# Optimization experiments

Measured on AMD Instinct MI355X. Metric: run time of the kernel, lower is better.

Reference implementation:

```python
import jax, jax.numpy as jnp
import numpy as np

B, SEQ, DIM, D, K = 32, 2048, 512, 512, 128


def _ln(x, g, b, eps=1e-5):
    m = x.mean(-1, keepdims=True)
    v = ((x - m) ** 2).mean(-1, keepdims=True)
    return (x - m) / jnp.sqrt(v + eps) * g + b


def _gelu(v):
    return jax.nn.gelu(v, approximate=False)


def _diff_topk(s, k, t):
    # s: (B, N) scores; iterative relaxed top-k (Xie & Ermon style).
    def step(carry, _):
        a = jax.nn.softmax(carry / t, axis=-1)
        carry = carry + jnp.log(jnp.clip(1.0 - a, 1e-6, 1.0))
        return carry, a
    _, Ws = jax.lax.scan(step, s, None, length=k)  # (k, B, N)
    return jnp.transpose(Ws, (1, 0, 2))            # (B, k, N)


def setup_inputs():
    key = jax.random.key(0)
    ks = jax.random.split(key, 6)
    w = lambda k_, shape: jax.random.normal(k_, shape, dtype=jnp.float32) * 0.02
    return {
        'x': jax.random.normal(ks[0], (B, SEQ, DIM), dtype=jnp.float32),
        'tau': jnp.array(0.0, dtype=jnp.float32),
        'ln1_g': jnp.ones((DIM,), jnp.float32), 'ln1_b': jnp.zeros((DIM,), jnp.float32),
        'W1': w(ks[1], (DIM, D)), 'b1': jnp.zeros((D,), jnp.float32),
        'ln2_g': jnp.ones((SEQ,), jnp.float32), 'ln2_b': jnp.zeros((SEQ,), jnp.float32),
        'W2': w(ks[2], (SEQ, SEQ)), 'b2': jnp.zeros((SEQ,), jnp.float32),
        'ln3_g': jnp.ones((D,), jnp.float32), 'ln3_b': jnp.zeros((D,), jnp.float32),
        'W3': w(ks[3], (D, D + 1)), 'b3': jnp.zeros((D + 1,), jnp.float32),
        'ln4_g': jnp.ones((D,), jnp.float32), 'ln4_b': jnp.zeros((D,), jnp.float32),
        'W4': w(ks[4], (D, DIM)), 'b4': jnp.zeros((DIM,), jnp.float32),
    }


def reference(x, tau, ln1_g, ln1_b, W1, b1, ln2_g, ln2_b, W2, b2,
              ln3_g, ln3_b, W3, b3, ln4_g, ln4_b, W4, b4):
    # tok_proj: LN(dim) -> Linear(dim, D) -> GELU
    x_tok = _gelu(_ln(x, ln1_g, ln1_b) @ W1 + b1)                  # (B, N, D)
    # ch_proj over the token axis: LN(seq) -> Linear(seq, seq) -> GELU
    xt = jnp.swapaxes(x_tok, 1, 2)                                  # (B, D, N)
    x_ch = jnp.swapaxes(_gelu(_ln(xt, ln2_g, ln2_b) @ W2 + b2), 1, 2)
    # proj -> split score | features
    h = _ln(x_tok + x_ch, ln3_g, ln3_b) @ W3 + b3                   # (B, N, D+1)
    x_score, x_proj = h[..., 0], h[..., 1:]
    t = jax.nn.sigmoid(jnp.clip(tau, -2.0, 5.0))
    Wmat = _diff_topk(x_score, K, t)                                # (B, k, N)
    Z = jnp.einsum('bkn,bnd->bkd', Wmat, x_proj)                    # soft gather
    Y = jnp.einsum('bkn,bkd->bnd', Wmat, Z)                         # soft scatter
    return _ln(x_proj + Y, ln4_g, ln4_b) @ W4 + b4                  # (B, N, dim)
```

## Files before the change

### kernel.cpp

```cpp
#include <hip/hip_runtime.h>
#include <math.h>

#define B_   32
#define SEQ_ 2048
#define DIM_ 512
#define KSEL 128

typedef _Float16 f16;
typedef _Float16 half8 __attribute__((ext_vector_type(8)));
typedef _Float16 half4 __attribute__((ext_vector_type(4)));
typedef float floatx4 __attribute__((ext_vector_type(4)));

#define LSTR2 32

__device__ __forceinline__ float gelu_exact(float v) {
  return 0.5f * v * (1.0f + erff(v * 0.70710678118654752440f));
}

__global__ __launch_bounds__(256) void rowstats512(const float* __restrict__ X,
                                                   float* __restrict__ mean,
                                                   float* __restrict__ rstd) {
  int row = blockIdx.x * 4 + (threadIdx.x >> 6);
  int l = threadIdx.x & 63;
  const float4* p = (const float4*)(X + (size_t)row * 512);
  float4 v0 = p[l * 2], v1 = p[l * 2 + 1];
  float s = v0.x + v0.y + v0.z + v0.w + v1.x + v1.y + v1.z + v1.w;
  float q = v0.x*v0.x + v0.y*v0.y + v0.z*v0.z + v0.w*v0.w
          + v1.x*v1.x + v1.y*v1.y + v1.z*v1.z + v1.w*v1.w;
#pragma unroll
  for (int off = 32; off > 0; off >>= 1) {
    s += __shfl_down(s, off);
    q += __shfl_down(q, off);
  }
  if (l == 0) {
    float m = s * (1.0f / 512.0f);
    float var = q * (1.0f / 512.0f) - m * m;
    mean[row] = m;
    rstd[row] = rsqrtf(var + 1e-5f);
  }
}

__global__ __launch_bounds__(256) void rowstats512_f16(const f16* __restrict__ X,
                                                       float* __restrict__ mean,
                                                       float* __restrict__ rstd) {
  int row = blockIdx.x * 4 + (threadIdx.x >> 6);
  int l = threadIdx.x & 63;
  half8 h = *(const half8*)(X + (size_t)row * 512 + l * 8);
  float s = 0.f, q = 0.f;
#pragma unroll
  for (int i = 0; i < 8; ++i) { float v = (float)h[i]; s += v; q += v * v; }
#pragma unroll
  for (int off = 32; off > 0; off >>= 1) {
    s += __shfl_down(s, off);
    q += __shfl_down(q, off);
  }
  if (l == 0) {
    float m = s * (1.0f / 512.0f);
    float var = q * (1.0f / 512.0f) - m * m;
    mean[row] = m;
    rstd[row] = rsqrtf(var + 1e-5f);
  }
}

__global__ __launch_bounds__(512) void colstats_part(const f16* __restrict__ xtok,
                                                     float2* __restrict__ part) {
  int b = blockIdx.x >> 3, pr = blockIdx.x & 7;
  int d = threadIdx.x;
  const f16* src = xtok + ((size_t)b * SEQ_ + (size_t)pr * 256) * 512 + d;
  float s = 0.f, q = 0.f;
#pragma unroll 4
  for (int i = 0; i < 256; ++i) {
    float v = (float)src[(size_t)i * 512];
    s += v; q += v * v;
  }
  part[(size_t)blockIdx.x * 512 + d] = make_float2(s, q);
}

__global__ __launch_bounds__(256) void colstats_fin(const float2* __restrict__ part,
                                                    float* __restrict__ mean,
                                                    float* __restrict__ rstd) {
  int idx = blockIdx.x * 256 + threadIdx.x;
  int b = idx >> 9;
  float s = 0.f, q = 0.f;
#pragma unroll
  for (int p = 0; p < 8; ++p) {
    float2 v = part[((size_t)(b * 8 + p)) * 512 + (idx & 511)];
    s += v.x; q += v.y;
  }
  float m = s * (1.0f / 2048.0f);
  mean[idx] = m;
  rstd[idx] = rsqrtf(q * (1.0f / 2048.0f) - m * m + 1e-5f);
}

template <typename T>
__global__ __launch_bounds__(256) void transpose_cvt(const T* __restrict__ src,
                                                     f16* __restrict__ dst,
                                                     int R, int C, long sb, long db) {
  __shared__ float tile[32][33];
  const T* s = src + (long)blockIdx.z * sb;
  f16* d = dst + (long)blockIdx.z * db;
  int c0 = blockIdx.x * 32, r0 = blockIdx.y * 32;
  int tx = threadIdx.x, ty = threadIdx.y;
#pragma unroll
  for (int i = 0; i < 4; ++i) {
    int r = r0 + ty + i * 8, c = c0 + tx;
    if (r < R && c < C) tile[ty + i * 8][tx] = (float)s[(long)r * C + c];
  }
  __syncthreads();
#pragma unroll
  for (int i = 0; i < 4; ++i) {
    int c = c0 + ty + i * 8, r = r0 + tx;
    if (c < C && r < R) d[(long)c * R + r] = (f16)tile[tx][ty + i * 8];
  }
}

__global__ __launch_bounds__(256) void trans2_kernel(const f16* __restrict__ xtok,
    const float* __restrict__ mean2, const float* __restrict__ rstd2,
    const float* __restrict__ g2, const float* __restrict__ bl2,
    f16* __restrict__ A2) {
  __shared__ float tile[32][33];
  int b = blockIdx.z;
  const f16* src = xtok + (long)b * SEQ_ * 512;
  f16* dst = A2 + (long)b * 512 * SEQ_;
  int d0 = blockIdx.x * 32, s0 = blockIdx.y * 32;
  int tx = threadIdx.x, ty = threadIdx.y;
  float m = mean2[b * 512 + d0 + tx];
  float rs = rstd2[b * 512 + d0 + tx];
#pragma unroll
  for (int i = 0; i < 4; ++i) {
    int s = s0 + ty + i * 8;
    float v = (float)src[(long)s * 512 + d0 + tx];
    tile[ty + i * 8][tx] = (v - m) * rs * g2[s] + bl2[s];
  }
  __syncthreads();
#pragma unroll
  for (int i = 0; i < 4; ++i) {
    int d = d0 + ty + i * 8, s = s0 + tx;
    dst[(long)d * SEQ_ + s] = (f16)tile[tx][ty + i * 8];
  }
}

__device__ __forceinline__ void stage_gll(const f16* __restrict__ src, long ld,
                                          int row0, int k0, f16* S, int t) {
  int w = t >> 6, lane = t & 63;
  int r = lane >> 2, c8 = (lane & 3) * 8;
#pragma unroll
  for (int i = 0; i < 2; ++i) {
    int chunk = w * 2 + i;
    const f16* g = src + (long)(row0 + chunk * 16 + r) * ld + k0 + c8;
    f16* l = S + chunk * 16 * LSTR2;
    __builtin_amdgcn_global_load_lds(
        (const __attribute__((address_space(1))) void*)g,
        (__attribute__((address_space(3))) void*)l, 16, 0, 0);
  }
}

__device__ __forceinline__ void stage_a_ln_f32(const float* __restrict__ src, long ld,
    const float* __restrict__ mean, const float* __restrict__ rstd,
    const float* __restrict__ g, const float* __restrict__ bl,
    int row0, int k0, f16* S, int t) {
  int row = t >> 1, kc = (t & 1) * 16;
  int r = row0 + row, c = k0 + kc;
  float m = mean[r], sd = rstd[r];
  const float* p = src + (long)r * ld + c;
  float v[16], gv[16], bv[16];
#pragma unroll
  for (int i = 0; i < 4; ++i) {
    float4 q = ((const float4*)p)[i];
    v[i*4+0]=q.x; v[i*4+1]=q.y; v[i*4+2]=q.z; v[i*4+3]=q.w;
    float4 gq = ((const float4*)(g + c))[i];
    gv[i*4+0]=gq.x; gv[i*4+1]=gq.y; gv[i*4+2]=gq.z; gv[i*4+3]=gq.w;
    float4 bq = ((const float4*)(bl + c))[i];
    bv[i*4+0]=bq.x; bv[i*4+1]=bq.y; bv[i*4+2]=bq.z; bv[i*4+3]=bq.w;
  }
  half8 o0, o1;
#pragma unroll
  for (int i = 0; i < 8; ++i) {
    o0[i] = (f16)((v[i] - m) * sd * gv[i] + bv[i]);
    o1[i] = (f16)((v[i + 8] - m) * sd * gv[i + 8] + bv[i + 8]);
  }
  *(half8*)(S + row * LSTR2 + kc) = o0;
  *(half8*)(S + row * LSTR2 + kc + 8) = o1;
}

__device__ __forceinline__ void stage_a_ln_f16(const f16* __restrict__ src, long ld,
    const float* __restrict__ mean, const float* __restrict__ rstd,
    const float* __restrict__ g, const float* __restrict__ bl,
    int row0, int k0, f16* S, int t) {
  int row = t >> 1, kc = (t & 1) * 16;
  int r = row0 + row, c = k0 + kc;
  float m = mean[r], sd = rstd[r];
  const f16* p = src + (long)r * ld + c;
  half8 h0 = *(const half8*)(p);
  half8 h1 = *(const half8*)(p + 8);
  float gv[16], bv[16];
#pragma unroll
  for (int i = 0; i < 4; ++i) {
    float4 gq = ((const float4*)(g + c))[i];
    gv[i*4+0]=gq.x; gv[i*4+1]=gq.y; gv[i*4+2]=gq.z; gv[i*4+3]=gq.w;
    float4 bq = ((const float4*)(bl + c))[i];
    bv[i*4+0]=bq.x; bv[i*4+1]=bq.y; bv[i*4+2]=bq.z; bv[i*4+3]=bq.w;
  }
  half8 o0, o1;
#pragma unroll
  for (int i = 0; i < 8; ++i) {
    o0[i] = (f16)(((float)h0[i] - m) * sd * gv[i] + bv[i]);
    o1[i] = (f16)(((float)h1[i] - m) * sd * gv[i + 8] + bv[i + 8]);
  }
  *(half8*)(S + row * LSTR2 + kc) = o0;
  *(half8*)(S + row * LSTR2 + kc + 8) = o1;
}

__device__ __forceinline__ void mfma_step(const f16* As, const f16* Bs, int lane,
                                          int wr, int wc, floatx4 acc[4][4]) {
  int kc = (lane >> 4) * 8;
  int rl = lane & 15;
  half8 a[4], b[4];
#pragma unroll
  for (int mi = 0; mi < 4; ++mi)
    a[mi] = *(const half8*)(As + (wr * 64 + mi * 16 + rl) * LSTR2 + kc);
#pragma unroll
  for (int ni = 0; ni < 4; ++ni)
    b[ni] = *(const half8*)(Bs + (wc * 64 + ni * 16 + rl) * LSTR2 + kc);
#pragma unroll
  for (int mi = 0; mi < 4; ++mi)
#pragma unroll
    for (int ni = 0; ni < 4; ++ni)
      acc[mi][ni] = __builtin_amdgcn_mfma_f32_16x16x32_f16(a[mi], b[ni], acc[mi][ni], 0, 0, 0);
}

#define GEMM_PROLOG \
  __shared__ __attribute__((aligned(16))) f16 As[128 * LSTR2]; \
  __shared__ __attribute__((aligned(16))) f16 Bs[128 * LSTR2]; \
  int t = threadIdx.x; \
  int lane = t & 63, w = t >> 6, wr = w >> 1, wc = w & 1; \
  floatx4 acc[4][4]; \
  _Pragma("unroll") for (int mi = 0; mi < 4; ++mi) \
  _Pragma("unroll") for (int ni = 0; ni < 4; ++ni) acc[mi][ni] = (floatx4){0.f,0.f,0.f,0.f};

__global__ __launch_bounds__(256) void g1_kernel(const float* __restrict__ x,
    const float* __restrict__ mean, const float* __restrict__ rstd,
    const float* __restrict__ g1, const float* __restrict__ bl1,
    const f16* __restrict__ W1T, const float* __restrict__ b1,
    f16* __restrict__ xtok) {
  GEMM_PROLOG
  int m0 = blockIdx.y * 128, n0 = blockIdx.x * 128;
  for (int k0 = 0; k0 < 512; k0 += 32) {
    stage_a_ln_f32(x, 512, mean, rstd, g1, bl1, m0, k0, As, t);
    stage_gll(W1T, 512, n0, k0, Bs, t);
    __syncthreads();
    mfma_step(As, Bs, lane, wr, wc, acc);
    __syncthreads();
  }
#pragma unroll
  for (int mi = 0; mi < 4; ++mi)
#pragma unroll
    for (int ni = 0; ni < 4; ++ni) {
      int c = n0 + wc * 64 + ni * 16 + (lane & 15);
      float bias = b1[c];
      int r0 = m0 + wr * 64 + mi * 16 + (lane >> 4) * 4;
#pragma unroll
      for (int j = 0; j < 4; ++j)
        xtok[(long)(r0 + j) * 512 + c] = (f16)gelu_exact(acc[mi][ni][j] + bias);
    }
}


__device__ __forceinline__ void stage_half(const f16* __restrict__ srcbase, long ld,
                                           f16* dst, int tid) {
#pragma unroll
  for (int q = 0; q < 2; ++q) {
    int row = q * 128 + (tid >> 2);
    int slot = (tid & 3) ^ ((row >> 1) & 3);
    const f16* g = srcbase + (long)row * ld + slot * 8;
    f16* lp = dst + (long)(q * 128 + (tid >> 6) * 16) * 32;
    __builtin_amdgcn_global_load_lds(
        (const __attribute__((address_space(1))) void*)g,
        (__attribute__((address_space(3))) void*)lp, 16, 0, 0);
  }
}

__device__ __forceinline__ half8 frag32(const f16* buf, int row, int sl) {
  return *(const half8*)(buf + (long)row * 32 + ((sl ^ ((row >> 1) & 3)) << 3));
}

#define BAR() __builtin_amdgcn_s_barrier()
#define WAITBAR4() do { asm volatile("s_waitcnt vmcnt(4)" ::: "memory"); \
                        __builtin_amdgcn_s_barrier(); } while (0)

__global__ __launch_bounds__(512, 2) void g2_8p(const f16* __restrict__ W2T,
    const f16* __restrict__ A2, const float* __restrict__ b2,
    const f16* __restrict__ xtok, f16* __restrict__ xsum) {
  __shared__ __attribute__((aligned(16))) f16 Ah[2][2][256 * 32];
  __shared__ __attribute__((aligned(16))) f16 Bh[2][2][256 * 32];
  int tid = threadIdx.x;
  int l = tid & 63, w = tid >> 6;
  int wr = w >> 2, wc = w & 3;
  int rl = l & 15, sl = l >> 4;
  int b = blockIdx.z;
  int m0 = blockIdx.y * 256;
  int n0 = blockIdx.x * 256;
  const f16* Am = W2T + (long)m0 * SEQ_;
  const f16* Bm = A2 + (long)b * 512 * SEQ_ + (long)n0 * SEQ_;
  const f16* xtb = xtok + (long)b * SEQ_ * 512;
  f16* xsb = xsum + (long)b * SEQ_ * 512;

  floatx4 acc[8][4];
#pragma unroll
  for (int mf = 0; mf < 8; ++mf)
#pragma unroll
    for (int nf = 0; nf < 4; ++nf) acc[mf][nf] = (floatx4){0.f, 0.f, 0.f, 0.f};

  half8 afr[4], bfr[4];

#define STAGE(base, tile, kk, dstbuf) \
  stage_half(base + (long)((tile) & 31) * 64 + (kk) * 32, SEQ_, dstbuf, tid)

#define READ_B(d, kk) \
  _Pragma("unroll") for (int nf = 0; nf < 4; ++nf) \
    bfr[nf] = frag32(Bh[d][kk], wc * 64 + nf * 16 + rl, sl);

#define READ_A(d, kk, mb) \
  _Pragma("unroll") for (int mi = 0; mi < 4; ++mi) \
    afr[mi] = frag32(Ah[d][kk], wr * 128 + ((mb) + mi) * 16 + rl, sl);

#define MFMA16(mb) \
  __builtin_amdgcn_s_setprio(1); \
  _Pragma("unroll") for (int mi = 0; mi < 4; ++mi) \
  _Pragma("unroll") for (int nf = 0; nf < 4; ++nf) \
    acc[(mb) + mi][nf] = __builtin_amdgcn_mfma_f32_16x16x32_f16(afr[mi], bfr[nf], acc[(mb) + mi][nf], 0, 0, 0); \
  __builtin_amdgcn_s_setprio(0);

  STAGE(Am, 0, 0, Ah[0][0]); STAGE(Am, 0, 1, Ah[0][1]);
  STAGE(Bm, 0, 0, Bh[0][0]); STAGE(Bm, 0, 1, Bh[0][1]);
  STAGE(Am, 1, 0, Ah[1][0]); STAGE(Bm, 1, 0, Bh[1][0]);
  asm volatile("s_waitcnt vmcnt(0)" ::: "memory");
  __builtin_amdgcn_s_barrier();

  for (int i = 0; i < 16; ++i) {
    STAGE(Am, 2 * i + 1, 1, Ah[1][1]);
    READ_B(0, 0); READ_A(0, 0, 0);
    BAR(); MFMA16(0); BAR();
    STAGE(Bm, 2 * i + 1, 1, Bh[1][1]);
    READ_A(0, 0, 4);
    BAR(); MFMA16(4); BAR();
    STAGE(Am, 2 * i + 2, 0, Ah[0][0]);
    READ_B(0, 1); READ_A(0, 1, 0);
    BAR(); MFMA16(0); BAR();
    STAGE(Bm, 2 * i + 2, 0, Bh[0][0]);
    READ_A(0, 1, 4);
    BAR(); MFMA16(4); WAITBAR4();
    STAGE(Am, 2 * i + 2, 1, Ah[0][1]);
    READ_B(1, 0); READ_A(1, 0, 0);
    BAR(); MFMA16(0); BAR();
    STAGE(Bm, 2 * i + 2, 1, Bh[0][1]);
    READ_A(1, 0, 4);
    BAR(); MFMA16(4); BAR();
    STAGE(Am, 2 * i + 3, 0, Ah[1][0]);
    READ_B(1, 1); READ_A(1, 1, 0);
    BAR(); MFMA16(0); BAR();
    STAGE(Bm, 2 * i + 3, 0, Bh[1][0]);
    READ_A(1, 1, 4);
    BAR(); MFMA16(4); WAITBAR4();
  }

#pragma unroll
  for (int mf = 0; mf < 8; ++mf) {
    int rbase = m0 + wr * 128 + mf * 16 + sl * 4;
#pragma unroll
    for (int j = 0; j < 4; ++j) {
      int r = rbase + j;
      float bias = b2[r];
      long rowoff = (long)r * 512;
#pragma unroll
      for (int nf = 0; nf < 4; ++nf) {
        int cc = n0 + wc * 64 + nf * 16 + rl;
        float v = gelu_exact(acc[mf][nf][j] + bias);
        xsb[rowoff + cc] = (f16)((float)xtb[rowoff + cc] + v);
      }
    }
  }
#undef STAGE
#undef READ_B
#undef READ_A
#undef MFMA16
}

__global__ __launch_bounds__(256) void g3_kernel(const f16* __restrict__ xsum,
    const float* __restrict__ mean, const float* __restrict__ rstd,
    const float* __restrict__ g3, const float* __restrict__ bl3,
    const f16* __restrict__ BT , const float* __restrict__ b3,
    f16* __restrict__ xproj, f16* __restrict__ xprojT) {
  GEMM_PROLOG
  int m0 = blockIdx.y * 128, n0 = blockIdx.x * 128;
  for (int k0 = 0; k0 < 512; k0 += 32) {
    stage_a_ln_f16(xsum, 512, mean, rstd, g3, bl3, m0, k0, As, t);
    stage_gll(BT, 512, n0, k0, Bs, t);
    __syncthreads();
    mfma_step(As, Bs, lane, wr, wc, acc);
    __syncthreads();
  }
#pragma unroll
  for (int mi = 0; mi < 4; ++mi)
#pragma unroll
    for (int ni = 0; ni < 4; ++ni) {
      int c = n0 + wc * 64 + ni * 16 + (lane & 15);
      float bias = b3[c + 1];
      int r0 = m0 + wr * 64 + mi * 16 + (lane >> 4) * 4;
      half4 xp;
#pragma unroll
      for (int j = 0; j < 4; ++j) {
        f16 v = (f16)(acc[mi][ni][j] + bias);
        xproj[(long)(r0 + j) * 512 + c] = v;
        xp[j] = v;
      }
      long bb = r0 >> 11;
      long rloc = r0 & 2047;
      *(half4*)(xprojT + (bb * 512 + c) * SEQ_ + rloc) = xp;
    }
}

__global__ __launch_bounds__(256) void score_kernel(const f16* __restrict__ xsum,
    const float* __restrict__ mean, const float* __restrict__ rstd,
    const float* __restrict__ g3, const float* __restrict__ bl3,
    const f16* __restrict__ w3c, const float* __restrict__ b3,
    float* __restrict__ xscore) {
  int row = blockIdx.x * 4 + (threadIdx.x >> 6);
  int l = threadIdx.x & 63;
  float m = mean[row], sd = rstd[row];
  half8 h = *(const half8*)(xsum + (long)row * 512 + l * 8);
  half8 wv = *(const half8*)(w3c + l * 8);
  float acc = 0.f;
#pragma unroll
  for (int i = 0; i < 8; ++i) {
    int d = l * 8 + i;
    float v = ((float)h[i] - m) * sd * g3[d] + bl3[d];
    acc += v * (float)wv[i];
  }
#pragma unroll
  for (int off = 32; off > 0; off >>= 1) acc += __shfl_down(acc, off);
  if (l == 0) xscore[row] = acc + b3[0];
}

__global__ __launch_bounds__(512) void topk_kernel(const float* __restrict__ xscore,
                                                   const float* __restrict__ tau,
                                                   f16* __restrict__ Wm) {
  int b = blockIdx.x, t = threadIdx.x;
  __shared__ float red[2][8];
  float tv = fminf(fmaxf(tau[0], -2.0f), 5.0f);
  float temp = 1.0f / (1.0f + expf(-tv));
  float it = 1.0f / temp;
  float c[4];
  const float* xs = xscore + (size_t)b * SEQ_;
  {
    float4 v = *(const float4*)(xs + t * 4);
    c[0] = v.x; c[1] = v.y; c[2] = v.z; c[3] = v.w;
  }
  int l = t & 63, wid = t >> 6;
  for (int k = 0; k < KSEL; ++k) {
    float e[4];
    float p = 0.f;
#pragma unroll
    for (int i = 0; i < 4; ++i) { e[i] = expf(c[i] * it); p += e[i]; }
#pragma unroll
    for (int off = 32; off > 0; off >>= 1) p += __shfl_down(p, off);
    if (l == 0) red[k & 1][wid] = p;
    __syncthreads();
    float S = 0.f;
#pragma unroll
    for (int q = 0; q < 8; ++q) S += red[k & 1][q];
    float iS = 1.0f / S;
    half4 h;
    float a[4];
#pragma unroll
    for (int i = 0; i < 4; ++i) { a[i] = e[i] * iS; h[i] = (f16)a[i]; }
    *(half4*)(Wm + ((size_t)b * KSEL + k) * SEQ_ + t * 4) = h;
#pragma unroll
    for (int i = 0; i < 4; ++i) c[i] += logf(fmaxf(1.0f - a[i], 1e-6f));
  }
}

__global__ __launch_bounds__(256) void gz_kernel(const f16* __restrict__ Wm,
    const f16* __restrict__ xprojT, float* __restrict__ Zpart) {
  GEMM_PROLOG
  int b = blockIdx.z, kc = blockIdx.y;
  int n0 = blockIdx.x * 128;
  const f16* A = Wm + (long)b * KSEL * SEQ_;
  const f16* BT = xprojT + (long)b * 512 * SEQ_;
  float* Zb = Zpart + ((long)b * 2 + kc) * KSEL * 512;
  int kbeg = kc * 1024, kend = kbeg + 1024;
  for (int k0 = kbeg; k0 < kend; k0 += 32) {
    stage_gll(A, SEQ_, 0, k0, As, t);
    stage_gll(BT, SEQ_, n0, k0, Bs, t);
    __syncthreads();
    mfma_step(As, Bs, lane, wr, wc, acc);
    __syncthreads();
  }
#pragma unroll
  for (int mi = 0; mi < 4; ++mi)
#pragma unroll
    for (int ni = 0; ni < 4; ++ni) {
      int c = n0 + wc * 64 + ni * 16 + (lane & 15);
      int r0 = wr * 64 + mi * 16 + (lane >> 4) * 4;
#pragma unroll
      for (int j = 0; j < 4; ++j)
        Zb[(long)(r0 + j) * 512 + c] = acc[mi][ni][j];
    }
}

__global__ __launch_bounds__(256) void ztrans_kernel(const float* __restrict__ Zpart,
                                                     f16* __restrict__ ZT) {
  __shared__ float tile[32][33];
  int b = blockIdx.z;
  int c0 = blockIdx.x * 32, r0 = blockIdx.y * 32;
  int tx = threadIdx.x, ty = threadIdx.y;
  const float* p0 = Zpart + ((long)b * 2 + 0) * KSEL * 512;
  const float* p1 = Zpart + ((long)b * 2 + 1) * KSEL * 512;
#pragma unroll
  for (int i = 0; i < 4; ++i) {
    int r = r0 + ty + i * 8, c = c0 + tx;
    tile[ty + i * 8][tx] = p0[(long)r * 512 + c] + p1[(long)r * 512 + c];
  }
  __syncthreads();
  f16* d = ZT + (long)b * 512 * KSEL;
#pragma unroll
  for (int i = 0; i < 4; ++i) {
    int c = c0 + ty + i * 8, r = r0 + tx;
    d[(long)c * KSEL + r] = (f16)tile[tx][ty + i * 8];
  }
}

__global__ __launch_bounds__(256) void gy_kernel(const f16* __restrict__ WmT,
    const f16* __restrict__ ZT, const f16* __restrict__ xproj,
    f16* __restrict__ rbuf) {
  GEMM_PROLOG
  int b = blockIdx.z;
  int m0 = blockIdx.y * 128, n0 = blockIdx.x * 128;
  const f16* A = WmT + (long)b * SEQ_ * KSEL;
  const f16* BT = ZT + (long)b * 512 * KSEL;
  const f16* xpb = xproj + (long)b * SEQ_ * 512;
  f16* rb = rbuf + (long)b * SEQ_ * 512;
  for (int k0 = 0; k0 < KSEL; k0 += 32) {
    stage_gll(A, KSEL, m0, k0, As, t);
    stage_gll(BT, KSEL, n0, k0, Bs, t);
    __syncthreads();
    mfma_step(As, Bs, lane, wr, wc, acc);
    __syncthreads();
  }
#pragma unroll
  for (int mi = 0; mi < 4; ++mi)
#pragma unroll
    for (int ni = 0; ni < 4; ++ni) {
      int c = n0 + wc * 64 + ni * 16 + (lane & 15);
      int r0 = m0 + wr * 64 + mi * 16 + (lane >> 4) * 4;
#pragma unroll
      for (int j = 0; j < 4; ++j) {
        long idx = (long)(r0 + j) * 512 + c;
        rb[idx] = (f16)((float)xpb[idx] + acc[mi][ni][j]);
      }
    }
}

__global__ __launch_bounds__(256) void g4_kernel(const f16* __restrict__ rbuf,
    const float* __restrict__ mean, const float* __restrict__ rstd,
    const float* __restrict__ g4, const float* __restrict__ bl4,
    const f16* __restrict__ W4T, const float* __restrict__ b4,
    float* __restrict__ out) {
  GEMM_PROLOG
  int m0 = blockIdx.y * 128, n0 = blockIdx.x * 128;
  for (int k0 = 0; k0 < 512; k0 += 32) {
    stage_a_ln_f16(rbuf, 512, mean, rstd, g4, bl4, m0, k0, As, t);
    stage_gll(W4T, 512, n0, k0, Bs, t);
    __syncthreads();
    mfma_step(As, Bs, lane, wr, wc, acc);
    __syncthreads();
  }
#pragma unroll
  for (int mi = 0; mi < 4; ++mi)
#pragma unroll
    for (int ni = 0; ni < 4; ++ni) {
      int c = n0 + wc * 64 + ni * 16 + (lane & 15);
      float bias = b4[c];
      int r0 = m0 + wr * 64 + mi * 16 + (lane >> 4) * 4;
#pragma unroll
      for (int j = 0; j < 4; ++j)
        out[(long)(r0 + j) * 512 + c] = acc[mi][ni][j] + bias;
    }
}

extern "C" void kernel_launch(void* const* d_in, const int* in_sizes, int n_in,
                              void* d_out, int out_size, void* d_ws, size_t ws_size,
                              hipStream_t stream) {
  const float* x    = (const float*)d_in[0];
  const float* tau  = (const float*)d_in[1];
  const float* g1   = (const float*)d_in[2];
  const float* bl1  = (const float*)d_in[3];
  const float* W1   = (const float*)d_in[4];
  const float* b1   = (const float*)d_in[5];
  const float* g2   = (const float*)d_in[6];
  const float* bl2  = (const float*)d_in[7];
  const float* W2   = (const float*)d_in[8];
  const float* b2   = (const float*)d_in[9];
  const float* g3   = (const float*)d_in[10];
  const float* bl3  = (const float*)d_in[11];
  const float* W3   = (const float*)d_in[12];
  const float* b3   = (const float*)d_in[13];
  const float* g4   = (const float*)d_in[14];
  const float* bl4  = (const float*)d_in[15];
  const float* W4   = (const float*)d_in[16];
  const float* b4   = (const float*)d_in[17];
  float* out = (float*)d_out;

  const long NTOK = (long)B_ * SEQ_;

  char* ws = (char*)d_ws;
  f16* regA   = (f16*)(ws);
  f16* regB   = (f16*)(ws + (64l << 20));
  float* Zpart = (float*)(ws + (128l << 20));
  f16* W2T    = (f16*)(ws + (144l << 20));
  f16* W1T    = (f16*)(ws + (152l << 20));
  f16* W3T    = (f16*)(ws + (153l << 20));
  f16* W4T    = (f16*)(ws + (154l << 20));
  float* xscore = (float*)(ws + (155l << 20));
  float* meanA  = (float*)(ws + (156l << 20));
  float* rstdA  = meanA + NTOK;
  float* mean2  = rstdA + NTOK;
  float* rstd2  = mean2 + B_ * 512;
  float2* part  = (float2*)(rstd2 + B_ * 512);
  f16* ZT     = (f16*)(ws + (157l << 20));

  f16* xtok   = (f16*)d_out;
  f16* xprojT = (f16*)d_out;
  f16* Wm     = (f16*)((char*)d_out + (64l << 20));
  f16* WmT    = (f16*)((char*)d_out + (80l << 20));

  f16* A2    = regA;
  f16* xsum  = regB;
  f16* xproj = regA;
  f16* rbuf  = regB;

  dim3 tb(32, 8);

  transpose_cvt<float><<<dim3(16, 16, 1), tb, 0, stream>>>(W1, W1T, 512, 512, 0, 0);
  transpose_cvt<float><<<dim3(64, 64, 1), tb, 0, stream>>>(W2, W2T, 2048, 2048, 0, 0);
  transpose_cvt<float><<<dim3(17, 16, 1), tb, 0, stream>>>(W3, W3T, 512, 513, 0, 0);
  transpose_cvt<float><<<dim3(16, 16, 1), tb, 0, stream>>>(W4, W4T, 512, 512, 0, 0);

  rowstats512<<<NTOK / 4, 256, 0, stream>>>(x, meanA, rstdA);
  g1_kernel<<<dim3(4, 512), 256, 0, stream>>>(x, meanA, rstdA, g1, bl1, W1T, b1, xtok);

  colstats_part<<<B_ * 8, 512, 0, stream>>>(xtok, part);
  colstats_fin<<<64, 256, 0, stream>>>(part, mean2, rstd2);
  trans2_kernel<<<dim3(16, 64, B_), tb, 0, stream>>>(xtok, mean2, rstd2, g2, bl2, A2);
  g2_8p<<<dim3(2, 8, B_), 512, 0, stream>>>(W2T, A2, b2, xtok, xsum);

  rowstats512_f16<<<NTOK / 4, 256, 0, stream>>>(xsum, meanA, rstdA);
  score_kernel<<<NTOK / 4, 256, 0, stream>>>(xsum, meanA, rstdA, g3, bl3, W3T, b3, xscore);
  g3_kernel<<<dim3(4, 512), 256, 0, stream>>>(xsum, meanA, rstdA, g3, bl3, W3T + 512, b3,
                                              xproj, xprojT);

  topk_kernel<<<B_, 512, 0, stream>>>(xscore, tau, Wm);

  transpose_cvt<f16><<<dim3(64, 4, B_), tb, 0, stream>>>(Wm, WmT, 128, 2048,
      (long)KSEL * SEQ_, (long)SEQ_ * KSEL);

  gz_kernel<<<dim3(4, 2, B_), 256, 0, stream>>>(Wm, xprojT, Zpart);
  ztrans_kernel<<<dim3(16, 4, B_), tb, 0, stream>>>(Zpart, ZT);

  gy_kernel<<<dim3(4, 16, B_), 256, 0, stream>>>(WmT, ZT, xproj, rbuf);

  rowstats512_f16<<<NTOK / 4, 256, 0, stream>>>(rbuf, meanA, rstdA);
  g4_kernel<<<dim3(4, 512), 256, 0, stream>>>(rbuf, meanA, rstdA, g4, bl4, W4T, b4, out);
}
```

Measured before the change: 876.2 us.

## Materialize LayerNorm outputs in f16 and load GEMM A tiles via LDS DMA

Replaces the stats-only row kernels before g1 and g4 with kernels that apply LayerNorm and write the normalized rows as f16. The GEMMs then stage their A tiles with global_load_lds, the same way they stage B, so the per-k-step LN arithmetic and the f32 loads of x (re-read once per N tile) leave the GEMM loop. This costs an extra f16 intermediate written and read through global memory. It also swaps the g2 grid's y and z axes so blocks that share the same W2T rows are scheduled next to each other, which should improve L2 reuse.

```diff
diff --git a/kernel.cpp b/kernel.cpp
--- a/kernel.cpp
+++ b/kernel.cpp
@@ -17,9 +17,9 @@
   return 0.5f * v * (1.0f + erff(v * 0.70710678118654752440f));
 }
 
-__global__ __launch_bounds__(256) void rowstats512(const float* __restrict__ X,
-                                                   float* __restrict__ mean,
-                                                   float* __restrict__ rstd) {
+__global__ __launch_bounds__(256) void ln_fuse_f32(const float* __restrict__ X,
+    const float* __restrict__ g, const float* __restrict__ bl,
+    f16* __restrict__ Y) {
   int row = blockIdx.x * 4 + (threadIdx.x >> 6);
   int l = threadIdx.x & 63;
   const float4* p = (const float4*)(X + (size_t)row * 512);
@@ -29,15 +29,58 @@
           + v1.x*v1.x + v1.y*v1.y + v1.z*v1.z + v1.w*v1.w;
 #pragma unroll
   for (int off = 32; off > 0; off >>= 1) {
-    s += __shfl_down(s, off);
-    q += __shfl_down(q, off);
-  }
-  if (l == 0) {
-    float m = s * (1.0f / 512.0f);
-    float var = q * (1.0f / 512.0f) - m * m;
-    mean[row] = m;
-    rstd[row] = rsqrtf(var + 1e-5f);
-  }
+    s += __shfl_xor(s, off);
+    q += __shfl_xor(q, off);
+  }
+  float m = s * (1.0f / 512.0f);
+  float sd = rsqrtf(q * (1.0f / 512.0f) - m * m + 1e-5f);
+  float4 g0 = ((const float4*)(g + l * 8))[0];
+  float4 g1v = ((const float4*)(g + l * 8))[1];
+  float4 b0 = ((const float4*)(bl + l * 8))[0];
+  float4 b1v = ((const float4*)(bl + l * 8))[1];
+  half8 o;
+  o[0] = (f16)((v0.x - m) * sd * g0.x + b0.x);
+  o[1] = (f16)((v0.y - m) * sd * g0.y + b0.y);
+  o[2] = (f16)((v0.z - m) * sd * g0.z + b0.z);
+  o[3] = (f16)((v0.w - m) * sd * g0.w + b0.w);
+  o[4] = (f16)((v1.x - m) * sd * g1v.x + b1v.x);
+  o[5] = (f16)((v1.y - m) * sd * g1v.y + b1v.y);
+  o[6] = (f16)((v1.z - m) * sd * g1v.z + b1v.z);
+  o[7] = (f16)((v1.w - m) * sd * g1v.w + b1v.w);
+  *(half8*)(Y + (size_t)row * 512 + l * 8) = o;
+}
+
+__global__ __launch_bounds__(256) void ln_fuse_f16(const f16* __restrict__ X,
+    const float* __restrict__ g, const float* __restrict__ bl,
+    f16* __restrict__ Y) {
+  int row = blockIdx.x * 4 + (threadIdx.x >> 6);
+  int l = threadIdx.x & 63;
+  half8 h = *(const half8*)(X + (size_t)row * 512 + l * 8);
+  float v[8];
+  float s = 0.f, q = 0.f;
+#pragma unroll
+  for (int i = 0; i < 8; ++i) { v[i] = (float)h[i]; s += v[i]; q += v[i] * v[i]; }
+#pragma unroll
+  for (int off = 32; off > 0; off >>= 1) {
+    s += __shfl_xor(s, off);
+    q += __shfl_xor(q, off);
+  }
+  float m = s * (1.0f / 512.0f);
+  float sd = rsqrtf(q * (1.0f / 512.0f) - m * m + 1e-5f);
+  float4 g0 = ((const float4*)(g + l * 8))[0];
+  float4 g1v = ((const float4*)(g + l * 8))[1];
+  float4 b0 = ((const float4*)(bl + l * 8))[0];
+  float4 b1v = ((const float4*)(bl + l * 8))[1];
+  half8 o;
+  o[0] = (f16)((v[0] - m) * sd * g0.x + b0.x);
+  o[1] = (f16)((v[1] - m) * sd * g0.y + b0.y);
+  o[2] = (f16)((v[2] - m) * sd * g0.z + b0.z);
+  o[3] = (f16)((v[3] - m) * sd * g0.w + b0.w);
+  o[4] = (f16)((v[4] - m) * sd * g1v.x + b1v.x);
+  o[5] = (f16)((v[5] - m) * sd * g1v.y + b1v.y);
+  o[6] = (f16)((v[6] - m) * sd * g1v.z + b1v.z);
+  o[7] = (f16)((v[7] - m) * sd * g1v.w + b1v.w);
+  *(half8*)(Y + (size_t)row * 512 + l * 8) = o;
 }
 
 __global__ __launch_bounds__(256) void rowstats512_f16(const f16* __restrict__ X,
@@ -155,34 +198,6 @@
   }
 }
 
-__device__ __forceinline__ void stage_a_ln_f32(const float* __restrict__ src, long ld,
-    const float* __restrict__ mean, const float* __restrict__ rstd,
-    const float* __restrict__ g, const float* __restrict__ bl,
-    int row0, int k0, f16* S, int t) {
-  int row = t >> 1, kc = (t & 1) * 16;
-  int r = row0 + row, c = k0 + kc;
-  float m = mean[r], sd = rstd[r];
-  const float* p = src + (long)r * ld + c;
-  float v[16], gv[16], bv[16];
-#pragma unroll
-  for (int i = 0; i < 4; ++i) {
-    float4 q = ((const float4*)p)[i];
-    v[i*4+0]=q.x; v[i*4+1]=q.y; v[i*4+2]=q.z; v[i*4+3]=q.w;
-    float4 gq = ((const float4*)(g + c))[i];
-    gv[i*4+0]=gq.x; gv[i*4+1]=gq.y; gv[i*4+2]=gq.z; gv[i*4+3]=gq.w;
-    float4 bq = ((const float4*)(bl + c))[i];
-    bv[i*4+0]=bq.x; bv[i*4+1]=bq.y; bv[i*4+2]=bq.z; bv[i*4+3]=bq.w;
-  }
-  half8 o0, o1;
-#pragma unroll
-  for (int i = 0; i < 8; ++i) {
-    o0[i] = (f16)((v[i] - m) * sd * gv[i] + bv[i]);
-    o1[i] = (f16)((v[i + 8] - m) * sd * gv[i + 8] + bv[i + 8]);
-  }
-  *(half8*)(S + row * LSTR2 + kc) = o0;
-  *(half8*)(S + row * LSTR2 + kc + 8) = o1;
-}
-
 __device__ __forceinline__ void stage_a_ln_f16(const f16* __restrict__ src, long ld,
     const float* __restrict__ mean, const float* __restrict__ rstd,
     const float* __restrict__ g, const float* __restrict__ bl,
@@ -238,15 +253,13 @@
   _Pragma("unroll") for (int mi = 0; mi < 4; ++mi) \
   _Pragma("unroll") for (int ni = 0; ni < 4; ++ni) acc[mi][ni] = (floatx4){0.f,0.f,0.f,0.f};
 
-__global__ __launch_bounds__(256) void g1_kernel(const float* __restrict__ x,
-    const float* __restrict__ mean, const float* __restrict__ rstd,
-    const float* __restrict__ g1, const float* __restrict__ bl1,
+__global__ __launch_bounds__(256) void g1_kernel(const f16* __restrict__ xln1,
     const f16* __restrict__ W1T, const float* __restrict__ b1,
     f16* __restrict__ xtok) {
   GEMM_PROLOG
   int m0 = blockIdx.y * 128, n0 = blockIdx.x * 128;
   for (int k0 = 0; k0 < 512; k0 += 32) {
-    stage_a_ln_f32(x, 512, mean, rstd, g1, bl1, m0, k0, As, t);
+    stage_gll(xln1, 512, m0, k0, As, t);
     stage_gll(W1T, 512, n0, k0, Bs, t);
     __syncthreads();
     mfma_step(As, Bs, lane, wr, wc, acc);
@@ -264,7 +277,6 @@
         xtok[(long)(r0 + j) * 512 + c] = (f16)gelu_exact(acc[mi][ni][j] + bias);
     }
 }
-
 
 __device__ __forceinline__ void stage_half(const f16* __restrict__ srcbase, long ld,
                                            f16* dst, int tid) {
@@ -297,8 +309,8 @@
   int l = tid & 63, w = tid >> 6;
   int wr = w >> 2, wc = w & 3;
   int rl = l & 15, sl = l >> 4;
-  int b = blockIdx.z;
-  int m0 = blockIdx.y * 256;
+  int b = blockIdx.y;
+  int m0 = blockIdx.z * 256;
   int n0 = blockIdx.x * 256;
   const f16* Am = W2T + (long)m0 * SEQ_;
   const f16* Bm = A2 + (long)b * 512 * SEQ_ + (long)n0 * SEQ_;
@@ -561,15 +573,13 @@
     }
 }
 
-__global__ __launch_bounds__(256) void g4_kernel(const f16* __restrict__ rbuf,
-    const float* __restrict__ mean, const float* __restrict__ rstd,
-    const float* __restrict__ g4, const float* __restrict__ bl4,
+__global__ __launch_bounds__(256) void g4_kernel(const f16* __restrict__ xln4,
     const f16* __restrict__ W4T, const float* __restrict__ b4,
     float* __restrict__ out) {
   GEMM_PROLOG
   int m0 = blockIdx.y * 128, n0 = blockIdx.x * 128;
   for (int k0 = 0; k0 < 512; k0 += 32) {
-    stage_a_ln_f16(rbuf, 512, mean, rstd, g4, bl4, m0, k0, As, t);
+    stage_gll(xln4, 512, m0, k0, As, t);
     stage_gll(W4T, 512, n0, k0, Bs, t);
     __syncthreads();
     mfma_step(As, Bs, lane, wr, wc, acc);
@@ -630,6 +640,7 @@
   f16* ZT     = (f16*)(ws + (157l << 20));
 
   f16* xtok   = (f16*)d_out;
+  f16* xln1   = (f16*)((char*)d_out + (64l << 20));
   f16* xprojT = (f16*)d_out;
   f16* Wm     = (f16*)((char*)d_out + (64l << 20));
   f16* WmT    = (f16*)((char*)d_out + (80l << 20));
@@ -638,6 +649,7 @@
   f16* xsum  = regB;
   f16* xproj = regA;
   f16* rbuf  = regB;
+  f16* xln4  = regA;
 
   dim3 tb(32, 8);
 
@@ -646,13 +658,13 @@
   transpose_cvt<float><<<dim3(17, 16, 1), tb, 0, stream>>>(W3, W3T, 512, 513, 0, 0);
   transpose_cvt<float><<<dim3(16, 16, 1), tb, 0, stream>>>(W4, W4T, 512, 512, 0, 0);
 
-  rowstats512<<<NTOK / 4, 256, 0, stream>>>(x, meanA, rstdA);
-  g1_kernel<<<dim3(4, 512), 256, 0, stream>>>(x, meanA, rstdA, g1, bl1, W1T, b1, xtok);
+  ln_fuse_f32<<<NTOK / 4, 256, 0, stream>>>(x, g1, bl1, xln1);
+  g1_kernel<<<dim3(4, 512), 256, 0, stream>>>(xln1, W1T, b1, xtok);
 
   colstats_part<<<B_ * 8, 512, 0, stream>>>(xtok, part);
   colstats_fin<<<64, 256, 0, stream>>>(part, mean2, rstd2);
   trans2_kernel<<<dim3(16, 64, B_), tb, 0, stream>>>(xtok, mean2, rstd2, g2, bl2, A2);
-  g2_8p<<<dim3(2, 8, B_), 512, 0, stream>>>(W2T, A2, b2, xtok, xsum);
+  g2_8p<<<dim3(2, 32, 8), 512, 0, stream>>>(W2T, A2, b2, xtok, xsum);
 
   rowstats512_f16<<<NTOK / 4, 256, 0, stream>>>(xsum, meanA, rstdA);
   score_kernel<<<NTOK / 4, 256, 0, stream>>>(xsum, meanA, rstdA, g3, bl3, W3T, b3, xscore);
@@ -669,6 +681,6 @@
 
   gy_kernel<<<dim3(4, 16, B_), 256, 0, stream>>>(WmT, ZT, xproj, rbuf);
 
-  rowstats512_f16<<<NTOK / 4, 256, 0, stream>>>(rbuf, meanA, rstdA);
-  g4_kernel<<<dim3(4, 512), 256, 0, stream>>>(rbuf, meanA, rstdA, g4, bl4, W4T, b4, out);
-}
+  ln_fuse_f16<<<NTOK / 4, 256, 0, stream>>>(rbuf, g4, bl4, xln4);
+  g4_kernel<<<dim3(4, 512), 256, 0, stream>>>(xln4, W4T, b4, out);
+}
```

Result: faster. 824.0 us (-6.0%).
